# Optimization experiments

Hardware: AMD Instinct MI355X
Metric: run time of the kernel (lower is better)

Reference implementation:

```python
import jax, jax.numpy as jnp
import numpy as np

B, L, D, H, MEM, POL = 32, 256, 768, 12, 384, 3
DK = D // H
ALPHA, BETA, GAMA = 1.0, 0.25, 0.1


def _forward(sequence_output, pooled_output, adj_reshape, src_mask, aspect_mask,
             ln_g, ln_b, wq, bq, wk, bk, wd, bd, weight_m, bias_m,
             wa0, ba0, wa1, ba1, ws0, bs0, ws1, bs1, affine1, affine2, wc, bc):
    b, l, d = sequence_output.shape
    h = weight_m.shape[0]
    dk = d // h

    # custom LayerNorm (torch std is unbiased, ddof=1)
    mu = sequence_output.mean(-1, keepdims=True)
    sd = jnp.std(sequence_output, axis=-1, keepdims=True, ddof=1)
    x = ln_g * (sequence_output - mu) / (sd + 1e-6) + ln_b  # gcn_inputs (dropout = eval identity)

    aspect_outs = x * aspect_mask[:, :, None]

    # multi-head projections  [B,H,L,dk]
    q = (x @ wq + bq).reshape(b, l, h, dk).transpose(0, 2, 1, 3)
    k = (x @ wk + bk).reshape(b, l, h, dk).transpose(0, 2, 1, 3)
    asp = aspect_outs @ wd + bd                       # [B,L,dk]
    asp = jnp.broadcast_to(asp[:, None], (b, h, l, dk))

    # aspect-conditioned scores: tanh(aspect @ W_m @ K^T + b_m)   [B,H,L,L]
    asps = jnp.tanh(jnp.einsum('bhld,hde,bhme->bhlm', asp, weight_m, k) + bias_m[0])
    avg = asps.sum(axis=-2) / l                       # [B,H,L]

    # fusion overwrite: for each aspect index idx, row idx and col idx <- avg.
    # Sequential loop semantics (ascending idx, row-then-col) collapse to:
    #   both aspect (i,j): value = avg[min(i,j)];  row-only: avg[j];  col-only: avg[i]
    is_asp = aspect_mask > 0                          # [B,L]
    rowm = is_asp[:, None, :, None]
    colm = is_asp[:, None, None, :]
    avg_i = avg[..., :, None]                         # [B,H,L,1]
    avg_j = avg[..., None, :]                         # [B,H,1,L]
    ge = (jnp.arange(l)[:, None] >= jnp.arange(l)[None, :])  # i>=j -> min=j
    both_val = jnp.where(ge, avg_j, avg_i)
    aspect_scores = jnp.where(rowm & colm, both_val,
                      jnp.where(rowm, avg_j,
                        jnp.where(colm, avg_i, asps)))

    # standard scaled-dot attention
    scores = jnp.einsum('bhld,bhmd->bhlm', q, k) / jnp.sqrt(jnp.float32(dk))
    scores = jnp.where(src_mask[:, None, None, :] == 0, -1e9, scores)
    s_attn = jax.nn.softmax(scores, axis=-1)          # dropout = eval identity

    aspect_score_avg = aspect_scores.mean(axis=1)     # [B,L,L]
    adj_s = s_attn.mean(axis=1)                       # [B,L,L]

    eye = jnp.eye(l, dtype=adj_s.dtype)
    adj_s = adj_s * (1.0 - eye) + eye                 # zero diag then add identity
    adj_s = src_mask[:, :, None] * adj_s

    adj_r = jnp.exp(ALPHA * adj_reshape)
    dist_mask = aspect_score_avg > BETA
    adj_r = jnp.where(dist_mask, 1.0, adj_r)
    adj_ag = adj_r * aspect_score_avg

    log_p = jax.nn.log_softmax(adj_ag, axis=-1)
    log_q = jax.nn.log_softmax(adj_s, axis=-1)
    q_t = jnp.exp(log_q)
    kl = jnp.sum(q_t * (log_q - log_p))
    kl_loss = jnp.exp(-1.0 * kl * GAMA)

    denom_s = adj_s.sum(axis=2, keepdims=True) + 1.0
    denom_ag = adj_ag.sum(axis=2, keepdims=True) + 1.0

    out_ag, out_s = x, x
    was = [(wa0, ba0), (wa1, ba1)]
    wss = [(ws0, bs0), (ws1, bs1)]
    for li in range(2):
        g_ag = jax.nn.relu(((adj_ag @ out_ag) @ was[li][0] + was[li][1]) / denom_ag)
        g_s = jax.nn.relu(((adj_s @ out_s) @ wss[li][0] + wss[li][1]) / denom_s)
        A1 = jax.nn.softmax(jnp.einsum('bld,de,bme->blm', g_ag, affine1, g_s), axis=-1)
        A2 = jax.nn.softmax(jnp.einsum('bld,de,bme->blm', g_s, affine2, g_ag), axis=-1)
        out_ag = A1 @ g_s
        out_s = A2 @ g_ag   # gcn_drop = eval identity

    asp_wn = aspect_mask.sum(axis=1, keepdims=True)   # [B,1]
    m = aspect_mask[:, :, None]
    outputs1 = (out_ag * m).sum(axis=1) / asp_wn      # [B,MEM]
    outputs2 = (out_s * m).sum(axis=1) / asp_wn

    final = jnp.concatenate([outputs1, outputs2, pooled_output], axis=-1) @ wc + bc
    return final, kl_loss


def setup_inputs() -> dict:
    key = jax.random.key(0)
    ks = jax.random.split(key, 16)
    s = 0.02
    pos = jnp.arange(L)
    start = 5 + (jnp.arange(B) % 16)
    aspect_mask = ((pos[None, :] >= start[:, None]) & (pos[None, :] < start[:, None] + 3)).astype(jnp.float32)
    f32 = jnp.float32
    return {
        'sequence_output': jax.random.normal(ks[0], (B, L, D), f32),
        'pooled_output': jax.random.normal(ks[1], (B, D), f32),
        'adj_reshape': jax.random.uniform(ks[2], (B, L, L), f32),
        'src_mask': jnp.ones((B, L), f32),
        'aspect_mask': aspect_mask,
        'ln_g': jnp.ones((D,), f32), 'ln_b': jnp.zeros((D,), f32),
        'wq': jax.random.normal(ks[3], (D, D), f32) * s, 'bq': jnp.zeros((D,), f32),
        'wk': jax.random.normal(ks[4], (D, D), f32) * s, 'bk': jnp.zeros((D,), f32),
        'wd': jax.random.normal(ks[5], (D, DK), f32) * s, 'bd': jnp.zeros((DK,), f32),
        'weight_m': jax.random.normal(ks[6], (H, DK, DK), f32) * s,
        'bias_m': jnp.zeros((1,), f32),
        'wa0': jax.random.normal(ks[7], (D, MEM), f32) * s, 'ba0': jnp.zeros((MEM,), f32),
        'wa1': jax.random.normal(ks[8], (MEM, MEM), f32) * s, 'ba1': jnp.zeros((MEM,), f32),
        'ws0': jax.random.normal(ks[9], (D, MEM), f32) * s, 'bs0': jnp.zeros((MEM,), f32),
        'ws1': jax.random.normal(ks[10], (MEM, MEM), f32) * s, 'bs1': jnp.zeros((MEM,), f32),
        'affine1': jax.random.normal(ks[11], (MEM, MEM), f32) * s,
        'affine2': jax.random.normal(ks[12], (MEM, MEM), f32) * s,
        'wc': jax.random.normal(ks[13], (2 * D, POL), f32) * s, 'bc': jnp.zeros((POL,), f32),
    }


def reference(sequence_output, pooled_output, adj_reshape, src_mask, aspect_mask,
              ln_g, ln_b, wq, bq, wk, bk, wd, bd, weight_m, bias_m,
              wa0, ba0, wa1, ba1, ws0, bs0, ws1, bs1, affine1, affine2, wc, bc):
    return _forward(sequence_output, pooled_output, adj_reshape, src_mask, aspect_mask,
                    ln_g, ln_b, wq, bq, wk, bk, wd, bd, weight_m, bias_m,
                    wa0, ba0, wa1, ba1, ws0, bs0, ws1, bs1, affine1, affine2, wc, bc)
```

## Files before the change

kernel.cpp:

```cpp
#include <hip/hip_runtime.h>

#define B_ 32
#define L_ 256
#define D_ 768
#define H_ 12
#define DK_ 64
#define MEM_ 384

typedef __attribute__((ext_vector_type(8))) short bfrag8;
typedef __attribute__((ext_vector_type(8))) unsigned short us8;
typedef __attribute__((ext_vector_type(4))) float f32x4;

__device__ inline unsigned short f2bf(float f) {
  unsigned u = __float_as_uint(f);
  return (unsigned short)((u + 0x7fffu + ((u >> 16) & 1u)) >> 16);
}
__device__ inline float bf2f(unsigned short u) {
  return __uint_as_float(((unsigned)u) << 16);
}
__device__ inline float tanh_fast(float x) {
  x = fminf(fmaxf(x, -30.f), 30.f);
  float e = __expf(2.f * x);
  return (e - 1.f) * __builtin_amdgcn_rcpf(e + 1.f);
}
__device__ inline void gload_lds16(const unsigned short* g, unsigned short* l) {
  __builtin_amdgcn_global_load_lds(
      (__attribute__((address_space(1))) void*)(g),
      (__attribute__((address_space(3))) void*)(l), 16, 0, 0);
}

__device__ inline float waveRedSum(float v) {
#pragma unroll
  for (int o = 32; o; o >>= 1) v += __shfl_xor(v, o, 64);
  return v;
}
__device__ inline float waveRedMax(float v) {
#pragma unroll
  for (int o = 32; o; o >>= 1) v = fmaxf(v, __shfl_xor(v, o, 64));
  return v;
}
__device__ inline float blkRedSum(float v, float* red) {
  v = waveRedSum(v);
  int w = threadIdx.x >> 6;
  __syncthreads();
  if ((threadIdx.x & 63) == 0) red[w] = v;
  __syncthreads();
  return red[0] + red[1] + red[2] + red[3];
}
__device__ inline float blkRedMax(float v, float* red) {
  v = waveRedMax(v);
  int w = threadIdx.x >> 6;
  __syncthreads();
  if ((threadIdx.x & 63) == 0) red[w] = v;
  __syncthreads();
  return fmaxf(fmaxf(red[0], red[1]), fmaxf(red[2], red[3]));
}

__global__ __launch_bounds__(256) void prep_kernel(
    const float* __restrict__ seq, const float* __restrict__ lng,
    const float* __restrict__ lnb, float* __restrict__ xout,
    unsigned short* __restrict__ xbf,
    const float* __restrict__ wq, unsigned short* __restrict__ wqT,
    const float* __restrict__ wk, unsigned short* __restrict__ wkT,
    const float* __restrict__ wa0, unsigned short* __restrict__ wa0T,
    const float* __restrict__ ws0, unsigned short* __restrict__ ws0T,
    const float* __restrict__ wa1, unsigned short* __restrict__ wa1T,
    const float* __restrict__ ws1, unsigned short* __restrict__ ws1T,
    const float* __restrict__ aff1, unsigned short* __restrict__ aff1T,
    const float* __restrict__ aff2, unsigned short* __restrict__ aff2T,
    const float* __restrict__ wd, unsigned short* __restrict__ wdT,
    const float* __restrict__ wm, unsigned short* __restrict__ wmT) {
  int bid = blockIdx.x;
  if (bid >= 600) {
    long row = bid - 600;
    const float* p = seq + row * D_;
    float v[3];
#pragma unroll
    for (int i = 0; i < 3; ++i) v[i] = p[threadIdx.x + i * 256];
    __shared__ float red[4];
    float s = v[0] + v[1] + v[2];
    s = blkRedSum(s, red);
    float mu = s * (1.f / D_);
    float ss = 0.f;
#pragma unroll
    for (int i = 0; i < 3; ++i) { float d = v[i] - mu; ss += d * d; }
    ss = blkRedSum(ss, red);
    float sd = sqrtf(ss * (1.f / (D_ - 1)));
    float inv = 1.f / (sd + 1e-6f);
#pragma unroll
    for (int i = 0; i < 3; ++i) {
      int c = threadIdx.x + i * 256;
      float o = lng[c] * (v[i] - mu) * inv + lnb[c];
      xout[row * D_ + c] = o;
      xbf[row * D_ + c] = f2bf(o);
    }
    return;
  }
  const float* src; unsigned short* dst; int Rr, Cc, tIdx;
  if (bid < 144)      { src = wq;   dst = wqT;   Rr = 768; Cc = 768; tIdx = bid; }
  else if (bid < 288) { src = wk;   dst = wkT;   Rr = 768; Cc = 768; tIdx = bid - 144; }
  else if (bid < 360) { src = wa0;  dst = wa0T;  Rr = 768; Cc = 384; tIdx = bid - 288; }
  else if (bid < 432) { src = ws0;  dst = ws0T;  Rr = 768; Cc = 384; tIdx = bid - 360; }
  else if (bid < 468) { src = wa1;  dst = wa1T;  Rr = 384; Cc = 384; tIdx = bid - 432; }
  else if (bid < 504) { src = ws1;  dst = ws1T;  Rr = 384; Cc = 384; tIdx = bid - 468; }
  else if (bid < 540) { src = aff1; dst = aff1T; Rr = 384; Cc = 384; tIdx = bid - 504; }
  else if (bid < 576) { src = aff2; dst = aff2T; Rr = 384; Cc = 384; tIdx = bid - 540; }
  else if (bid < 588) { src = wd;   dst = wdT;   Rr = 768; Cc = 64;  tIdx = bid - 576; }
  else { int h = bid - 588; src = wm + h * 4096; dst = wmT + h * 4096; Rr = 64; Cc = 64; tIdx = 0; }
  __shared__ float tile[64][65];
  int nx = Cc >> 6;
  int c0 = (tIdx % nx) * 64, r0 = (tIdx / nx) * 64;
  int tx = threadIdx.x & 63, ty = threadIdx.x >> 6;
#pragma unroll
  for (int i = 0; i < 16; ++i)
    tile[ty + i * 4][tx] = src[(long)(r0 + ty + i * 4) * Cc + c0 + tx];
  __syncthreads();
#pragma unroll
  for (int i = 0; i < 16; ++i)
    dst[(long)(c0 + ty + i * 4) * Rr + r0 + tx] = f2bf(tile[tx][ty + i * 4]);
}

template <int MR>
__global__ __launch_bounds__(256) void gemm_bb(
    const unsigned short* __restrict__ A, const unsigned short* __restrict__ Bt,
    float* __restrict__ C, unsigned short* __restrict__ Cbf,
    unsigned short* __restrict__ CT,
    int M, int N, int K, long sA, long sB, long sC, long sCT,
    const float* __restrict__ bias, const float* __restrict__ rowDiv, int relu,
    const unsigned short* __restrict__ A2, const unsigned short* __restrict__ Bt2,
    float* __restrict__ C2, unsigned short* __restrict__ Cbf2,
    unsigned short* __restrict__ CT2,
    const float* __restrict__ bias2, const float* __restrict__ rowDiv2, int zsplit) {
  constexpr int MFRAG = MR / 32;
  constexpr int RW = MR / 2;
  constexpr int ASH = MR * 32;
  constexpr int TSH = 64 * (MR + 8);
  constexpr int SMN = (ASH + 4096 > TSH) ? (ASH + 4096) : TSH;
  __shared__ alignas(16) unsigned short smem[SMN];
  unsigned short* AsS = smem;
  unsigned short* BsS = smem + ASH;
  const int tid = threadIdx.x;
  const int bn = blockIdx.x, bm = blockIdx.y;
  int bz = blockIdx.z;
  const unsigned short* Ap = A; const unsigned short* Btp = Bt;
  float* Cp = C; unsigned short* Cbp = Cbf; unsigned short* CTp = CT;
  const float* biasp = bias; const float* rowDivp = rowDiv;
  if (zsplit > 0 && bz >= zsplit) {
    bz -= zsplit;
    Ap = A2; Btp = Bt2; Cp = C2; Cbp = Cbf2; CTp = CT2; biasp = bias2; rowDivp = rowDiv2;
  }
  Ap += (long)bz * sA; Btp += (long)bz * sB;
  if (Cp) Cp += (long)bz * sC;
  if (Cbp) Cbp += (long)bz * sC;
  if (CTp) CTp += (long)bz * sCT;

  f32x4 acc[MFRAG][4] = {};
  const int l = tid & 63, w = tid >> 6;
  const int wr = w >> 1, wc = w & 1;
  const int lr = l & 15, sg = l >> 4;

  const int rc = l >> 2;
  const int sslot = (l & 3) ^ ((rc >> 1) & 3);
  const unsigned short* gA0 = Ap + (long)(bm * MR + w * 16 + rc) * K + sslot * 8;
  const unsigned short* gA1 = (MR == 128)
      ? Ap + (long)(bm * MR + (w + 4) * 16 + rc) * K + sslot * 8 : nullptr;
  const unsigned short* gB0 = Btp + (long)(bn * 128 + w * 16 + rc) * K + sslot * 8;
  const unsigned short* gB1 = Btp + (long)(bn * 128 + (w + 4) * 16 + rc) * K + sslot * 8;
  unsigned short* lA0 = AsS + w * 512;
  unsigned short* lA1 = AsS + (w + 4) * 512;
  unsigned short* lB0 = BsS + w * 512;
  unsigned short* lB1 = BsS + (w + 4) * 512;

  const int off = (sg ^ ((lr >> 1) & 3)) * 8;
  const unsigned short* arp[MFRAG];
  const unsigned short* brp[4];
#pragma unroll
  for (int m = 0; m < MFRAG; ++m)
    arp[m] = AsS + (wr * RW + m * 16 + lr) * 32 + off;
#pragma unroll
  for (int n = 0; n < 4; ++n)
    brp[n] = BsS + (wc * 64 + n * 16 + lr) * 32 + off;

  for (int k0 = 0; k0 < K; k0 += 32) {
    gload_lds16(gA0 + k0, lA0);
    if (MR == 128) gload_lds16(gA1 + k0, lA1);
    gload_lds16(gB0 + k0, lB0);
    gload_lds16(gB1 + k0, lB1);
    __syncthreads();
    bfrag8 af[MFRAG], bf[4];
#pragma unroll
    for (int m = 0; m < MFRAG; ++m) af[m] = *(const bfrag8*)(arp[m] + 0);
#pragma unroll
    for (int n = 0; n < 4; ++n) bf[n] = *(const bfrag8*)(brp[n] + 0);
#pragma unroll
    for (int m = 0; m < MFRAG; ++m)
#pragma unroll
      for (int n = 0; n < 4; ++n)
        acc[m][n] = __builtin_amdgcn_mfma_f32_16x16x32_bf16(af[m], bf[n], acc[m][n], 0, 0, 0);
    __syncthreads();
  }

  if (Cp || Cbp) {
#pragma unroll
    for (int m = 0; m < MFRAG; ++m) {
#pragma unroll
      for (int r = 0; r < 4; ++r) {
        int row = bm * MR + wr * RW + m * 16 + (l >> 4) * 4 + r;
        float rd = rowDivp ? 1.f / rowDivp[(long)bz * M + row] : 1.f;
#pragma unroll
        for (int n = 0; n < 4; ++n) {
          int col = bn * 128 + wc * 64 + n * 16 + lr;
          float v = acc[m][n][r];
          if (biasp) v += biasp[col];
          v *= rd;
          if (relu) v = fmaxf(v, 0.f);
          if (Cp) Cp[(long)row * N + col] = v;
          if (Cbp) Cbp[(long)row * N + col] = f2bf(v);
        }
      }
    }
  }
  if (CT) {
    auto Ts = (unsigned short(*)[MR + 8])smem;
#pragma unroll
    for (int ch = 0; ch < 2; ++ch) {
      __syncthreads();
      if (wc == ch) {
#pragma unroll
        for (int m = 0; m < MFRAG; ++m) {
#pragma unroll
          for (int r = 0; r < 4; ++r) {
            int rowl = wr * RW + m * 16 + (l >> 4) * 4 + r;
            float rd = rowDivp ? 1.f / rowDivp[(long)bz * M + bm * MR + rowl] : 1.f;
#pragma unroll
            for (int n = 0; n < 4; ++n) {
              int col = bn * 128 + wc * 64 + n * 16 + lr;
              float v = acc[m][n][r];
              if (biasp) v += biasp[col];
              v *= rd;
              if (relu) v = fmaxf(v, 0.f);
              Ts[n * 16 + lr][rowl] = f2bf(v);
            }
          }
        }
      }
      __syncthreads();
      int trow = tid >> 2, tc = (tid & 3) * (MR / 4);
      int colg = bn * 128 + ch * 64 + trow;
      int rowg = bm * MR + tc;
      unsigned short* dp = CTp + (long)(rowg >> 8) * sCT + (long)colg * 256 + (rowg & 255);
#pragma unroll
      for (int j = 0; j < MR / 32; ++j)
        *(us8*)(dp + j * 8) = *(const us8*)&Ts[trow][tc + j * 8];
    }
  }
}

__global__ __launch_bounds__(256) void attn_asp(
    const unsigned short* __restrict__ qbf, const unsigned short* __restrict__ kbf,
    const float* __restrict__ srcm, float* __restrict__ adj_s,
    unsigned short* __restrict__ adjsbf,
    const unsigned short* __restrict__ xbf, const unsigned short* __restrict__ wdT,
    const float* __restrict__ amask, const float* __restrict__ bd,
    unsigned short* __restrict__ aspbf) {
  int t = threadIdx.x;
  int w = t >> 6, l = t & 63;
  int lr = l & 15, kg = (l >> 4) * 8;
  if (blockIdx.x >= 512) {
    int l0 = (blockIdx.x - 512) << 4;
    const unsigned short* ap = xbf + (long)(l0 + lr) * D_ + kg;
    const unsigned short* bp = wdT + (long)(w * 16 + lr) * D_ + kg;
    f32x4 acc = {};
#pragma unroll
    for (int k0 = 0; k0 < D_; k0 += 32) {
      bfrag8 af = *(const bfrag8*)(ap + k0);
      bfrag8 bf = *(const bfrag8*)(bp + k0);
      acc = __builtin_amdgcn_mfma_f32_16x16x32_bf16(af, bf, acc, 0, 0, 0);
    }
    int col = w * 16 + lr;
#pragma unroll
    for (int r = 0; r < 4; ++r) {
      int row = l0 + (l >> 4) * 4 + r;
      float v = acc[r] * amask[row] + bd[col];
      aspbf[(long)row * DK_ + col] = f2bf(v);
    }
    return;
  }
  int blk = blockIdx.x;
  int b = blk >> 4, l0 = (blk & 15) << 4;
  int rbase = (l >> 4) * 4;
  __shared__ float red[6][2][16][8];
  float acc[4][4] = {};
  float cmv[4];
#pragma unroll
  for (int ct = 0; ct < 4; ++ct) cmv[ct] = srcm[b * L_ + w * 64 + ct * 16 + lr];

#pragma unroll 1
  for (int hp = 0; hp < 6; ++hp) {
    const unsigned short* ap = qbf + ((long)b * L_ + l0 + lr) * D_ + hp * 128 + kg;
    bfrag8 a00 = *(const bfrag8*)ap;
    bfrag8 a01 = *(const bfrag8*)(ap + 32);
    bfrag8 a10 = *(const bfrag8*)(ap + 64);
    bfrag8 a11 = *(const bfrag8*)(ap + 96);
    float sv0[4][4], sv1[4][4];
#pragma unroll
    for (int ct = 0; ct < 4; ++ct) {
      const unsigned short* bp =
          kbf + ((long)b * L_ + w * 64 + ct * 16 + lr) * D_ + hp * 128 + kg;
      bfrag8 b00 = *(const bfrag8*)bp;
      bfrag8 b01 = *(const bfrag8*)(bp + 32);
      bfrag8 b10 = *(const bfrag8*)(bp + 64);
      bfrag8 b11 = *(const bfrag8*)(bp + 96);
      f32x4 c0 = {}, c1 = {};
      c0 = __builtin_amdgcn_mfma_f32_16x16x32_bf16(a00, b00, c0, 0, 0, 0);
      c0 = __builtin_amdgcn_mfma_f32_16x16x32_bf16(a01, b01, c0, 0, 0, 0);
      c1 = __builtin_amdgcn_mfma_f32_16x16x32_bf16(a10, b10, c1, 0, 0, 0);
      c1 = __builtin_amdgcn_mfma_f32_16x16x32_bf16(a11, b11, c1, 0, 0, 0);
      bool msk = (cmv[ct] == 0.f);
#pragma unroll
      for (int r = 0; r < 4; ++r) {
        sv0[ct][r] = msk ? -1e9f : c0[r] * 0.125f;
        sv1[ct][r] = msk ? -1e9f : c1[r] * 0.125f;
      }
    }
    float mx0a[4], mx1a[4];
#pragma unroll
    for (int r = 0; r < 4; ++r) {
      float m0 = fmaxf(fmaxf(sv0[0][r], sv0[1][r]), fmaxf(sv0[2][r], sv0[3][r]));
      float m1 = fmaxf(fmaxf(sv1[0][r], sv1[1][r]), fmaxf(sv1[2][r], sv1[3][r]));
#pragma unroll
      for (int o = 1; o < 16; o <<= 1) {
        m0 = fmaxf(m0, __shfl_xor(m0, o, 64));
        m1 = fmaxf(m1, __shfl_xor(m1, o, 64));
      }
      mx0a[r] = m0; mx1a[r] = m1;
      float s0 = 0.f, s1 = 0.f;
#pragma unroll
      for (int ct = 0; ct < 4; ++ct) {
        float e0 = __expf(sv0[ct][r] - m0);
        float e1 = __expf(sv1[ct][r] - m1);
        sv0[ct][r] = e0; sv1[ct][r] = e1;
        s0 += e0; s1 += e1;
      }
#pragma unroll
      for (int o = 1; o < 16; o <<= 1) {
        s0 += __shfl_xor(s0, o, 64);
        s1 += __shfl_xor(s1, o, 64);
      }
      if (lr == 0) {
        red[hp][0][rbase + r][w] = m0;
        red[hp][0][rbase + r][4 + w] = s0;
        red[hp][1][rbase + r][w] = m1;
        red[hp][1][rbase + r][4 + w] = s1;
      }
    }
    __syncthreads();
#pragma unroll
    for (int r = 0; r < 4; ++r) {
      f32x4 m4 = *(const f32x4*)&red[hp][0][rbase + r][0];
      f32x4 s4 = *(const f32x4*)&red[hp][0][rbase + r][4];
      float mt = fmaxf(fmaxf(m4[0], m4[1]), fmaxf(m4[2], m4[3]));
      float tot = s4[0] * __expf(m4[0] - mt) + s4[1] * __expf(m4[1] - mt) +
                  s4[2] * __expf(m4[2] - mt) + s4[3] * __expf(m4[3] - mt);
      float sc0 = __expf(mx0a[r] - mt) * __builtin_amdgcn_rcpf(tot);
      f32x4 n4 = *(const f32x4*)&red[hp][1][rbase + r][0];
      f32x4 t4 = *(const f32x4*)&red[hp][1][rbase + r][4];
      float nt = fmaxf(fmaxf(n4[0], n4[1]), fmaxf(n4[2], n4[3]));
      float tt = t4[0] * __expf(n4[0] - nt) + t4[1] * __expf(n4[1] - nt) +
                 t4[2] * __expf(n4[2] - nt) + t4[3] * __expf(n4[3] - nt);
      float sc1 = __expf(mx1a[r] - nt) * __builtin_amdgcn_rcpf(tt);
#pragma unroll
      for (int ct = 0; ct < 4; ++ct)
        acc[ct][r] += sv0[ct][r] * sc0 + sv1[ct][r] * sc1;
    }
  }

#pragma unroll
  for (int r = 0; r < 4; ++r) {
    int row = l0 + rbase + r;
    float rm = srcm[b * L_ + row];
#pragma unroll
    for (int ct = 0; ct < 4; ++ct) {
      int col = w * 64 + ct * 16 + lr;
      float v = acc[ct][r] * (1.f / H_);
      if (col == row) v = 1.f;
      v *= rm;
      long idx = ((long)b * L_ + row) * L_ + col;
      adj_s[idx] = v;
      adjsbf[idx] = f2bf(v);
    }
  }
}

__global__ __launch_bounds__(256) void asp_wm_v2(const unsigned short* __restrict__ aspbf,
                                                 const unsigned short* __restrict__ wmT,
                                                 unsigned short* __restrict__ tmpA) {
  int bh = blockIdx.x;
  int b = bh / H_, h = bh % H_;
  int t = threadIdx.x;
  int w = t >> 6, l = t & 63;
  int lr = l & 15, kg = (l >> 4) * 8;
  const unsigned short* wp = wmT + h * 4096;
  f32x4 acc[4][4] = {};
#pragma unroll
  for (int ks = 0; ks < 2; ++ks) {
    int k0 = ks * 32;
    bfrag8 af[4], bf[4];
#pragma unroll
    for (int m = 0; m < 4; ++m)
      af[m] = *(const bfrag8*)(aspbf + (long)(b * L_ + w * 64 + m * 16 + lr) * DK_ + k0 + kg);
#pragma unroll
    for (int n = 0; n < 4; ++n)
      bf[n] = *(const bfrag8*)(wp + (n * 16 + lr) * 64 + k0 + kg);
#pragma unroll
    for (int m = 0; m < 4; ++m)
#pragma unroll
      for (int n = 0; n < 4; ++n)
        acc[m][n] = __builtin_amdgcn_mfma_f32_16x16x32_bf16(af[m], bf[n], acc[m][n], 0, 0, 0);
  }
#pragma unroll
  for (int m = 0; m < 4; ++m)
#pragma unroll
    for (int n = 0; n < 4; ++n)
#pragma unroll
      for (int r = 0; r < 4; ++r) {
        int row = w * 64 + m * 16 + (l >> 4) * 4 + r;
        int col = n * 16 + lr;
        tmpA[(((long)b * H_ + h) * L_ + row) * DK_ + col] = f2bf(acc[m][n][r]);
      }
}

__global__ __launch_bounds__(256) void gemm_sfmx(
    const unsigned short* __restrict__ u1, const unsigned short* __restrict__ g1,
    unsigned short* __restrict__ P1,
    const unsigned short* __restrict__ u2, const unsigned short* __restrict__ g2,
    unsigned short* __restrict__ P2) {
  int bm = blockIdx.x;
  int bz = blockIdx.y;
  const unsigned short* Ap; const unsigned short* Bp; unsigned short* Pp;
  if (bz < 32) {
    Ap = u1 + (long)bz * L_ * MEM_; Bp = g1 + (long)bz * L_ * MEM_;
    Pp = P1 + (long)bz * L_ * L_;
  } else {
    int z = bz - 32;
    Ap = u2 + (long)z * L_ * MEM_; Bp = g2 + (long)z * L_ * MEM_;
    Pp = P2 + (long)z * L_ * L_;
  }
  __shared__ unsigned short As[64][40];
  __shared__ unsigned short Bs[256][40];
  __shared__ float redm[2][64];
  __shared__ float reds[2][64];
  const int t = threadIdx.x;
  const int l = t & 63, w = t >> 6;
  const int wr = w >> 1, wc = w & 1;
  const int lr = l & 15, kg = (l >> 4) * 8;
  f32x4 acc[2][8] = {};
  const int arA = t >> 2, akA = (t & 3) * 8;

  for (int k0 = 0; k0 < MEM_; k0 += 32) {
    *(us8*)&As[arA][akA] = *(const us8*)(Ap + (long)(bm * 64 + arA) * MEM_ + k0 + akA);
#pragma unroll
    for (int j = 0; j < 4; ++j)
      *(us8*)&Bs[t][j * 8] = *(const us8*)(Bp + (long)t * MEM_ + k0 + j * 8);
    __syncthreads();
    bfrag8 af[2], bf[8];
#pragma unroll
    for (int m = 0; m < 2; ++m) af[m] = *(const bfrag8*)&As[wr * 32 + m * 16 + lr][kg];
#pragma unroll
    for (int n = 0; n < 8; ++n) bf[n] = *(const bfrag8*)&Bs[wc * 128 + n * 16 + lr][kg];
#pragma unroll
    for (int m = 0; m < 2; ++m)
#pragma unroll
      for (int n = 0; n < 8; ++n)
        acc[m][n] = __builtin_amdgcn_mfma_f32_16x16x32_bf16(af[m], bf[n], acc[m][n], 0, 0, 0);
    __syncthreads();
  }

#pragma unroll
  for (int m = 0; m < 2; ++m) {
#pragma unroll
    for (int r = 0; r < 4; ++r) {
      int lrow = wr * 32 + m * 16 + (l >> 4) * 4 + r;
      float mx = -1e30f;
#pragma unroll
      for (int n = 0; n < 8; ++n) mx = fmaxf(mx, acc[m][n][r]);
#pragma unroll
      for (int o = 1; o < 16; o <<= 1) mx = fmaxf(mx, __shfl_xor(mx, o, 64));
      if (lr == 0) redm[wc][lrow] = mx;
    }
  }
  __syncthreads();
#pragma unroll
  for (int m = 0; m < 2; ++m) {
#pragma unroll
    for (int r = 0; r < 4; ++r) {
      int lrow = wr * 32 + m * 16 + (l >> 4) * 4 + r;
      float mx = fmaxf(redm[0][lrow], redm[1][lrow]);
      float s = 0.f;
#pragma unroll
      for (int n = 0; n < 8; ++n) {
        float e = __expf(acc[m][n][r] - mx);
        acc[m][n][r] = e;
        s += e;
      }
#pragma unroll
      for (int o = 1; o < 16; o <<= 1) s += __shfl_xor(s, o, 64);
      if (lr == 0) reds[wc][lrow] = s;
    }
  }
  __syncthreads();
#pragma unroll
  for (int m = 0; m < 2; ++m) {
#pragma unroll
    for (int r = 0; r < 4; ++r) {
      int lrow = wr * 32 + m * 16 + (l >> 4) * 4 + r;
      float inv = 1.f / (reds[0][lrow] + reds[1][lrow]);
      int row = bm * 64 + lrow;
#pragma unroll
      for (int n = 0; n < 8; ++n) {
        int col = wc * 128 + n * 16 + lr;
        Pp[(long)row * L_ + col] = f2bf(acc[m][n][r] * inv);
      }
    }
  }
}

__global__ __launch_bounds__(256) void asps_mean_v2(
    const unsigned short* __restrict__ tmpA,
    const unsigned short* __restrict__ kbf,
    const float* __restrict__ bias_m,
    float* __restrict__ asps_mean) {
  int blk = blockIdx.x;
  int b = blk >> 4, l0 = (blk & 15) << 4;
  int t = threadIdx.x;
  int w = t >> 6, l = t & 63;
  int lr = l & 15, kg = (l >> 4) * 8;
  float bm = bias_m[0];
  float accg[4][4] = {};
  for (int h = 0; h < H_; ++h) {
    const unsigned short* ap = tmpA + (((long)b * H_ + h) * L_ + l0 + lr) * 64 + kg;
    bfrag8 af0 = *(const bfrag8*)ap;
    bfrag8 af1 = *(const bfrag8*)(ap + 32);
#pragma unroll
    for (int ct = 0; ct < 4; ++ct) {
      const unsigned short* bp =
          kbf + ((long)b * L_ + w * 64 + ct * 16 + lr) * D_ + h * 64 + kg;
      bfrag8 bf0 = *(const bfrag8*)bp;
      bfrag8 bf1 = *(const bfrag8*)(bp + 32);
      f32x4 accl = {};
      accl = __builtin_amdgcn_mfma_f32_16x16x32_bf16(af0, bf0, accl, 0, 0, 0);
      accl = __builtin_amdgcn_mfma_f32_16x16x32_bf16(af1, bf1, accl, 0, 0, 0);
#pragma unroll
      for (int r = 0; r < 4; ++r) accg[ct][r] += tanh_fast(accl[r] + bm);
    }
  }
#pragma unroll
  for (int ct = 0; ct < 4; ++ct) {
    int col = w * 64 + ct * 16 + lr;
#pragma unroll
    for (int r = 0; r < 4; ++r) {
      int row = l0 + (l >> 4) * 4 + r;
      asps_mean[((long)b * L_ + row) * L_ + col] = accg[ct][r] * (1.f / H_);
    }
  }
}

__global__ __launch_bounds__(1024) void avgh_kernel(const float* __restrict__ asps_mean,
                                                    float* __restrict__ avgH) {
  int b = blockIdx.x;
  int m = threadIdx.x & 255, q = threadIdx.x >> 8;
  __shared__ float part[4][256];
  float s = 0.f;
  for (int l = q * 64; l < q * 64 + 64; ++l)
    s += asps_mean[((long)b * L_ + l) * L_ + m];
  part[q][m] = s;
  __syncthreads();
  if (q == 0)
    avgH[b * L_ + m] = (part[0][m] + part[1][m] + part[2][m] + part[3][m]) * (1.f / L_);
}

__global__ __launch_bounds__(256) void adjag_kernel(const float* __restrict__ asps_mean,
                                                    const float* __restrict__ avgH,
                                                    const float* __restrict__ amask,
                                                    const float* __restrict__ adjr,
                                                    float* __restrict__ adj_ag,
                                                    unsigned short* __restrict__ adjagbf) {
  long idx = (long)blockIdx.x * 256 + threadIdx.x;
  int m = idx & 255;
  long bl = idx >> 8;
  int l = (int)(bl & 255);
  int b = (int)(bl >> 8);
  bool rowa = amask[b * L_ + l] > 0.f;
  bool cola = amask[b * L_ + m] > 0.f;
  float asa;
  if (rowa && cola) asa = (l >= m) ? avgH[b * L_ + m] : avgH[b * L_ + l];
  else if (rowa)    asa = avgH[b * L_ + m];
  else if (cola)    asa = avgH[b * L_ + l];
  else              asa = asps_mean[idx];
  float r = (asa > 0.25f) ? 1.f : expf(adjr[idx]);
  float v = r * asa;
  adj_ag[idx] = v;
  adjagbf[idx] = f2bf(v);
}

__global__ __launch_bounds__(256) void kl_denom(const float* __restrict__ adj_s,
                                                const float* __restrict__ adj_ag,
                                                float* __restrict__ klpart,
                                                float* __restrict__ den_s,
                                                float* __restrict__ den_ag) {
  long row = blockIdx.x;
  int m = threadIdx.x;
  __shared__ float red[4];
  float s = adj_s[row * L_ + m];
  float a = adj_ag[row * L_ + m];
  float sum_s = blkRedSum(s, red);
  float sum_a = blkRedSum(a, red);
  float mx_s = blkRedMax(s, red);
  float mx_a = blkRedMax(a, red);
  float es = expf(s - mx_s), ea = expf(a - mx_a);
  float ses = blkRedSum(es, red);
  float sea = blkRedSum(ea, red);
  float logq = (s - mx_s) - logf(ses);
  float logp = (a - mx_a) - logf(sea);
  float term = (es / ses) * (logq - logp);
  float kp = blkRedSum(term, red);
  if (m == 0) {
    klpart[row] = kp;
    den_s[row] = sum_s + 1.f;
    den_ag[row] = sum_a + 1.f;
  }
}

__global__ __launch_bounds__(256) void kl_final(const float* __restrict__ klpart,
                                                float* __restrict__ dout) {
  __shared__ float red[4];
  float s = 0.f;
  for (int i = threadIdx.x; i < B_ * L_; i += 256) s += klpart[i];
  s = blkRedSum(s, red);
  if (threadIdx.x == 0) dout[96] = expf(-s * 0.1f);
}

__global__ __launch_bounds__(256) void final_kernel(const unsigned short* __restrict__ o_ag,
                                                    const unsigned short* __restrict__ o_s,
                                                    const float* __restrict__ pooled,
                                                    const float* __restrict__ amask,
                                                    const float* __restrict__ wc,
                                                    const float* __restrict__ bc,
                                                    float* __restrict__ dout) {
  int b = blockIdx.x, t = threadIdx.x;
  __shared__ float cS[1536];
  __shared__ float maskS[256];
  __shared__ float red[4];
  maskS[t] = amask[b * L_ + t];
  float wn = blkRedSum(maskS[t], red);
  for (int e = t; e < MEM_; e += 256) {
    float s1 = 0.f, s2 = 0.f;
    for (int l = 0; l < L_; ++l) {
      float mk = maskS[l];
      if (mk != 0.f) {
        s1 += mk * bf2f(o_ag[((long)b * L_ + l) * MEM_ + e]);
        s2 += mk * bf2f(o_s[((long)b * L_ + l) * MEM_ + e]);
      }
    }
    cS[e] = s1 / wn;
    cS[MEM_ + e] = s2 / wn;
  }
  for (int j = t; j < D_; j += 256) cS[2 * MEM_ + j] = pooled[b * D_ + j];
  __syncthreads();
  float p0 = 0.f, p1 = 0.f, p2 = 0.f;
  for (int j = t; j < 1536; j += 256) {
    float v = cS[j];
    p0 += v * wc[j * 3 + 0];
    p1 += v * wc[j * 3 + 1];
    p2 += v * wc[j * 3 + 2];
  }
  p0 = blkRedSum(p0, red);
  p1 = blkRedSum(p1, red);
  p2 = blkRedSum(p2, red);
  if (t == 0) {
    dout[b * 3 + 0] = p0 + bc[0];
    dout[b * 3 + 1] = p1 + bc[1];
    dout[b * 3 + 2] = p2 + bc[2];
  }
}

extern "C" void kernel_launch(void* const* d_in, const int* in_sizes, int n_in,
                              void* d_out, int out_size, void* d_ws, size_t ws_size,
                              hipStream_t stream) {
  const float* seq    = (const float*)d_in[0];
  const float* pooled = (const float*)d_in[1];
  const float* adjr   = (const float*)d_in[2];
  const float* srcm   = (const float*)d_in[3];
  const float* amask  = (const float*)d_in[4];
  const float* ln_g   = (const float*)d_in[5];
  const float* ln_b   = (const float*)d_in[6];
  const float* wq     = (const float*)d_in[7];
  const float* bq     = (const float*)d_in[8];
  const float* wk     = (const float*)d_in[9];
  const float* bk     = (const float*)d_in[10];
  const float* wd     = (const float*)d_in[11];
  const float* bd     = (const float*)d_in[12];
  const float* wm     = (const float*)d_in[13];
  const float* bm     = (const float*)d_in[14];
  const float* wa0    = (const float*)d_in[15];
  const float* ba0    = (const float*)d_in[16];
  const float* wa1    = (const float*)d_in[17];
  const float* ba1    = (const float*)d_in[18];
  const float* ws0    = (const float*)d_in[19];
  const float* bs0    = (const float*)d_in[20];
  const float* ws1    = (const float*)d_in[21];
  const float* bs1    = (const float*)d_in[22];
  const float* aff1   = (const float*)d_in[23];
  const float* aff2   = (const float*)d_in[24];
  const float* wc     = (const float*)d_in[25];
  const float* bc     = (const float*)d_in[26];

  float* ws = (float*)d_ws;
  float* S0 = ws;
  float* S1 = S0 + 6291456;
  float* S2 = S1 + 3145728;
  float* S3 = S2 + 3145728;
  float* S4 = S3 + 3145728;
  float* S5 = S4 + 524288;
  float* adj_s  = S5 + 2097152;
  float* adj_ag = adj_s + 2097152;
  unsigned short* adjsbf  = (unsigned short*)(adj_ag + 2097152);
  unsigned short* adjagbf = adjsbf + 2097152;
  unsigned short* wT      = adjagbf + 2097152;
  unsigned short* wqT   = wT;
  unsigned short* wkT   = wT + 589824;
  unsigned short* wa0T  = wT + 1179648;
  unsigned short* ws0T  = wT + 1474560;
  unsigned short* wa1T  = wT + 1769472;
  unsigned short* ws1T  = wT + 1916928;
  unsigned short* aff1T = wT + 2064384;
  unsigned short* aff2T = wT + 2211840;
  float* tail   = (float*)(wT + 2359296);
  float* avgH   = tail;
  float* den_s  = avgH + 8192;
  float* den_ag = den_s + 8192;
  float* klp    = den_ag + 8192;

  float* x = S0;
  unsigned short* o_agbf = (unsigned short*)S0;
  unsigned short* o_sbf  = o_agbf + 3145728;
  unsigned short* gTag   = o_agbf + 6291456;
  unsigned short* gTs    = o_agbf + 9437184;
  unsigned short* xbf    = (unsigned short*)S1;
  unsigned short* qbf    = (unsigned short*)S2;
  unsigned short* tmpA   = (unsigned short*)S2;
  unsigned short* g_agbf = (unsigned short*)S2;
  unsigned short* g_sbf  = g_agbf + 3145728;
  unsigned short* kbf    = (unsigned short*)S3;
  unsigned short* tTag   = (unsigned short*)S3;
  unsigned short* tTs    = tTag + 3145728;
  unsigned short* u1bf   = (unsigned short*)S3;
  unsigned short* u2bf   = u1bf + 3145728;
  unsigned short* aspbf  = (unsigned short*)S4;
  unsigned short* wdT    = aspbf + 524288;
  unsigned short* wmT    = wdT + 49152;
  float* asps = S5;
  unsigned short* P1bf = (unsigned short*)S5;
  unsigned short* P2bf = P1bf + 2097152;
  float* dout = (float*)d_out;

  const long sAdjSh = (long)L_ * L_;
  const long sMemSh = (long)L_ * MEM_;

  prep_kernel<<<600 + B_ * L_, 256, 0, stream>>>(
      seq, ln_g, ln_b, x, xbf, wq, wqT, wk, wkT, wa0, wa0T, ws0, ws0T,
      wa1, wa1T, ws1, ws1T, aff1, aff1T, aff2, aff2T, wd, wdT, wm, wmT);
  gemm_bb<128><<<dim3(6, 64, 2), 256, 0, stream>>>(
      xbf, wqT, nullptr, qbf, nullptr, 8192, 768, 768, 0, 0, 0, 0, bq, nullptr, 0,
      xbf, wkT, nullptr, kbf, nullptr, bk, nullptr, 1);
  attn_asp<<<1024, 256, 0, stream>>>(qbf, kbf, srcm, adj_s, adjsbf,
                                     xbf, wdT, amask, bd, aspbf);
  asp_wm_v2<<<B_ * H_, 256, 0, stream>>>(aspbf, wmT, tmpA);
  asps_mean_v2<<<B_ * 16, 256, 0, stream>>>(tmpA, kbf, bm, asps);
  avgh_kernel<<<B_, 1024, 0, stream>>>(asps, avgH);
  adjag_kernel<<<B_ * L_ * L_ / 256, 256, 0, stream>>>(asps, avgH, amask, adjr,
                                                       adj_ag, adjagbf);
  kl_denom<<<B_ * L_, 256, 0, stream>>>(adj_s, adj_ag, klp, den_s, den_ag);
  kl_final<<<1, 256, 0, stream>>>(klp, dout);

  for (int li = 0; li < 2; ++li) {
    int Kd = li ? MEM_ : D_;
    const unsigned short* inag = li ? o_agbf : xbf;
    const unsigned short* ins  = li ? o_sbf : xbf;
    const unsigned short* wAT = li ? wa1T : wa0T;
    const float* bA = li ? ba1 : ba0;
    const unsigned short* wST = li ? ws1T : ws0T;
    const float* bS = li ? bs1 : bs0;
    gemm_bb<64><<<dim3(3, 128, 2), 256, 0, stream>>>(
        inag, wAT, nullptr, nullptr, tTag, 8192, MEM_, Kd, 0, 0, 0, sMemSh,
        nullptr, nullptr, 0,
        ins, wST, nullptr, nullptr, tTs, nullptr, nullptr, 1);
    gemm_bb<64><<<dim3(3, 4, 64), 256, 0, stream>>>(
        adjagbf, tTag, nullptr, g_agbf, gTag, L_, MEM_, L_, sAdjSh, sMemSh, sMemSh,
        sMemSh, bA, den_ag, 1,
        adjsbf, tTs, nullptr, g_sbf, gTs, bS, den_s, 32);
    gemm_bb<64><<<dim3(3, 128, 2), 256, 0, stream>>>(
        g_agbf, aff1T, nullptr, u1bf, nullptr, 8192, MEM_, MEM_, 0, 0, 0, 0,
        nullptr, nullptr, 0,
        g_sbf, aff2T, nullptr, u2bf, nullptr, nullptr, nullptr, 1);
    gemm_sfmx<<<dim3(4, 64), 256, 0, stream>>>(u1bf, g_sbf, P1bf, u2bf, g_agbf, P2bf);
    gemm_bb<64><<<dim3(3, 4, 64), 256, 0, stream>>>(
        P1bf, gTs, nullptr, o_agbf, nullptr, L_, MEM_, L_, sAdjSh, sMemSh, sMemSh, 0,
        nullptr, nullptr, 0,
        P2bf, gTag, nullptr, o_sbf, nullptr, nullptr, nullptr, 32);
  }

  final_kernel<<<B_, 256, 0, stream>>>(o_agbf, o_sbf, pooled, amask, wc, bc, dout);
}
```

Measured before the change: 432.7 us.

## Fuse adj_ag construction with KL, fold KL final into final kernel, retile QK GEMM

Merges the adjacency-aggregation kernel with the per-row KL/denominator kernel so adj_ag is consumed from registers instead of re-read from memory. The single-block KL final reduction becomes an extra block of final_kernel, removing a launch. The Q/K projection GEMM switches from 128 to 64 tiles with twice the grid, and attn_asp hoists all K fragment loads ahead of the MFMAs to give more memory-level parallelism at the cost of more registers.

```diff
diff --git a/kernel.cpp b/kernel.cpp
--- a/kernel.cpp
+++ b/kernel.cpp
@@ -302,20 +302,24 @@
     bfrag8 a01 = *(const bfrag8*)(ap + 32);
     bfrag8 a10 = *(const bfrag8*)(ap + 64);
     bfrag8 a11 = *(const bfrag8*)(ap + 96);
-    float sv0[4][4], sv1[4][4];
+    bfrag8 kv[4][4];
 #pragma unroll
     for (int ct = 0; ct < 4; ++ct) {
       const unsigned short* bp =
           kbf + ((long)b * L_ + w * 64 + ct * 16 + lr) * D_ + hp * 128 + kg;
-      bfrag8 b00 = *(const bfrag8*)bp;
-      bfrag8 b01 = *(const bfrag8*)(bp + 32);
-      bfrag8 b10 = *(const bfrag8*)(bp + 64);
-      bfrag8 b11 = *(const bfrag8*)(bp + 96);
+      kv[ct][0] = *(const bfrag8*)bp;
+      kv[ct][1] = *(const bfrag8*)(bp + 32);
+      kv[ct][2] = *(const bfrag8*)(bp + 64);
+      kv[ct][3] = *(const bfrag8*)(bp + 96);
+    }
+    float sv0[4][4], sv1[4][4];
+#pragma unroll
+    for (int ct = 0; ct < 4; ++ct) {
       f32x4 c0 = {}, c1 = {};
-      c0 = __builtin_amdgcn_mfma_f32_16x16x32_bf16(a00, b00, c0, 0, 0, 0);
-      c0 = __builtin_amdgcn_mfma_f32_16x16x32_bf16(a01, b01, c0, 0, 0, 0);
-      c1 = __builtin_amdgcn_mfma_f32_16x16x32_bf16(a10, b10, c1, 0, 0, 0);
-      c1 = __builtin_amdgcn_mfma_f32_16x16x32_bf16(a11, b11, c1, 0, 0, 0);
+      c0 = __builtin_amdgcn_mfma_f32_16x16x32_bf16(a00, kv[ct][0], c0, 0, 0, 0);
+      c0 = __builtin_amdgcn_mfma_f32_16x16x32_bf16(a01, kv[ct][1], c0, 0, 0, 0);
+      c1 = __builtin_amdgcn_mfma_f32_16x16x32_bf16(a10, kv[ct][2], c1, 0, 0, 0);
+      c1 = __builtin_amdgcn_mfma_f32_16x16x32_bf16(a11, kv[ct][3], c1, 0, 0, 0);
       bool msk = (cmv[ct] == 0.f);
 #pragma unroll
       for (int r = 0; r < 4; ++r) {
@@ -579,17 +583,21 @@
     avgH[b * L_ + m] = (part[0][m] + part[1][m] + part[2][m] + part[3][m]) * (1.f / L_);
 }
 
-__global__ __launch_bounds__(256) void adjag_kernel(const float* __restrict__ asps_mean,
-                                                    const float* __restrict__ avgH,
-                                                    const float* __restrict__ amask,
-                                                    const float* __restrict__ adjr,
-                                                    float* __restrict__ adj_ag,
-                                                    unsigned short* __restrict__ adjagbf) {
-  long idx = (long)blockIdx.x * 256 + threadIdx.x;
-  int m = idx & 255;
-  long bl = idx >> 8;
-  int l = (int)(bl & 255);
-  int b = (int)(bl >> 8);
+__global__ __launch_bounds__(256) void adjag_kl(const float* __restrict__ asps_mean,
+                                                const float* __restrict__ avgH,
+                                                const float* __restrict__ amask,
+                                                const float* __restrict__ adjr,
+                                                const float* __restrict__ adj_s,
+                                                float* __restrict__ adj_ag,
+                                                unsigned short* __restrict__ adjagbf,
+                                                float* __restrict__ klpart,
+                                                float* __restrict__ den_s,
+                                                float* __restrict__ den_ag) {
+  long row = blockIdx.x;
+  int m = threadIdx.x;
+  int l = (int)(row & 255);
+  int b = (int)(row >> 8);
+  long idx = row * L_ + m;
   bool rowa = amask[b * L_ + l] > 0.f;
   bool cola = amask[b * L_ + m] > 0.f;
   float asa;
@@ -598,21 +606,12 @@
   else if (cola)    asa = avgH[b * L_ + l];
   else              asa = asps_mean[idx];
   float r = (asa > 0.25f) ? 1.f : expf(adjr[idx]);
-  float v = r * asa;
-  adj_ag[idx] = v;
-  adjagbf[idx] = f2bf(v);
-}
-
-__global__ __launch_bounds__(256) void kl_denom(const float* __restrict__ adj_s,
-                                                const float* __restrict__ adj_ag,
-                                                float* __restrict__ klpart,
-                                                float* __restrict__ den_s,
-                                                float* __restrict__ den_ag) {
-  long row = blockIdx.x;
-  int m = threadIdx.x;
+  float a = r * asa;
+  adj_ag[idx] = a;
+  adjagbf[idx] = f2bf(a);
+
   __shared__ float red[4];
-  float s = adj_s[row * L_ + m];
-  float a = adj_ag[row * L_ + m];
+  float s = adj_s[idx];
   float sum_s = blkRedSum(s, red);
   float sum_a = blkRedSum(a, red);
   float mx_s = blkRedMax(s, red);
@@ -631,26 +630,25 @@
   }
 }
 
-__global__ __launch_bounds__(256) void kl_final(const float* __restrict__ klpart,
-                                                float* __restrict__ dout) {
-  __shared__ float red[4];
-  float s = 0.f;
-  for (int i = threadIdx.x; i < B_ * L_; i += 256) s += klpart[i];
-  s = blkRedSum(s, red);
-  if (threadIdx.x == 0) dout[96] = expf(-s * 0.1f);
-}
-
 __global__ __launch_bounds__(256) void final_kernel(const unsigned short* __restrict__ o_ag,
                                                     const unsigned short* __restrict__ o_s,
                                                     const float* __restrict__ pooled,
                                                     const float* __restrict__ amask,
                                                     const float* __restrict__ wc,
                                                     const float* __restrict__ bc,
+                                                    const float* __restrict__ klpart,
                                                     float* __restrict__ dout) {
   int b = blockIdx.x, t = threadIdx.x;
+  __shared__ float red[4];
+  if (b == B_) {
+    float s = 0.f;
+    for (int i = t; i < B_ * L_; i += 256) s += klpart[i];
+    s = blkRedSum(s, red);
+    if (t == 0) dout[96] = expf(-s * 0.1f);
+    return;
+  }
   __shared__ float cS[1536];
   __shared__ float maskS[256];
-  __shared__ float red[4];
   maskS[t] = amask[b * L_ + t];
   float wn = blkRedSum(maskS[t], red);
   for (int e = t; e < MEM_; e += 256) {
@@ -770,7 +768,7 @@
   prep_kernel<<<600 + B_ * L_, 256, 0, stream>>>(
       seq, ln_g, ln_b, x, xbf, wq, wqT, wk, wkT, wa0, wa0T, ws0, ws0T,
       wa1, wa1T, ws1, ws1T, aff1, aff1T, aff2, aff2T, wd, wdT, wm, wmT);
-  gemm_bb<128><<<dim3(6, 64, 2), 256, 0, stream>>>(
+  gemm_bb<64><<<dim3(6, 128, 2), 256, 0, stream>>>(
       xbf, wqT, nullptr, qbf, nullptr, 8192, 768, 768, 0, 0, 0, 0, bq, nullptr, 0,
       xbf, wkT, nullptr, kbf, nullptr, bk, nullptr, 1);
   attn_asp<<<1024, 256, 0, stream>>>(qbf, kbf, srcm, adj_s, adjsbf,
@@ -778,10 +776,8 @@
   asp_wm_v2<<<B_ * H_, 256, 0, stream>>>(aspbf, wmT, tmpA);
   asps_mean_v2<<<B_ * 16, 256, 0, stream>>>(tmpA, kbf, bm, asps);
   avgh_kernel<<<B_, 1024, 0, stream>>>(asps, avgH);
-  adjag_kernel<<<B_ * L_ * L_ / 256, 256, 0, stream>>>(asps, avgH, amask, adjr,
-                                                       adj_ag, adjagbf);
-  kl_denom<<<B_ * L_, 256, 0, stream>>>(adj_s, adj_ag, klp, den_s, den_ag);
-  kl_final<<<1, 256, 0, stream>>>(klp, dout);
+  adjag_kl<<<B_ * L_, 256, 0, stream>>>(asps, avgH, amask, adjr, adj_s,
+                                        adj_ag, adjagbf, klp, den_s, den_ag);
 
   for (int li = 0; li < 2; ++li) {
     int Kd = li ? MEM_ : D_;
@@ -810,5 +806,6 @@
         P2bf, gTag, nullptr, o_sbf, nullptr, nullptr, nullptr, 32);
   }
 
-  final_kernel<<<B_, 256, 0, stream>>>(o_agbf, o_sbf, pooled, amask, wc, bc, dout);
-}
+  final_kernel<<<B_ + 1, 256, 0, stream>>>(o_agbf, o_sbf, pooled, amask, wc, bc,
+                                           klp, dout);
+}
```

Result: no change. 429.1 us (-0.8%).
